# Performance work log

Measured on AMD Instinct MI355X. Metric: run time of the kernel, lower is better.

## Reference

```python
import jax, jax.numpy as jnp
import numpy as np

B, S, E = 2, 2048, 4096
H, KVH, D = 32, 8, 128          # query heads, kv heads, head_dim
GROUPS = H // KVH               # 4
WINDOW = 4096                   # sliding window (>= S -> fully causal)
ROPE_THETA = 10000.0


def _rope_sin_cos(position_ids):
    # inv_freq over even dims, freqs duplicated (Mixtral/GPT-NeoX style)
    inv_freq = 1.0 / (ROPE_THETA ** (jnp.arange(0, D, 2, dtype=jnp.float32) / D))  # [D/2]
    freqs = position_ids.astype(jnp.float32)[..., None] * inv_freq  # [B,S,D/2]
    emb = jnp.concatenate((freqs, freqs), axis=-1)                  # [B,S,D]
    # add head axis for broadcasting against [B,S,H,D]
    return jnp.sin(emb)[:, :, None, :], jnp.cos(emb)[:, :, None, :]


def _rotate_half(x):
    return jnp.concatenate((-x[..., D // 2:], x[..., :D // 2]), axis=-1)


def setup_inputs() -> dict:
    key = jax.random.key(0)
    ks = jax.random.split(key, 5)
    w_scale = 1.0 / np.sqrt(E)
    hidden_states = jax.random.normal(ks[0], (B, S, E), jnp.float32)
    Wq = jax.random.normal(ks[1], (E, H * D), jnp.float32) * w_scale
    Wk = jax.random.normal(ks[2], (E, KVH * D), jnp.float32) * w_scale
    Wv = jax.random.normal(ks[3], (E, KVH * D), jnp.float32) * w_scale
    Wo = jax.random.normal(ks[4], (H * D, E), jnp.float32) * w_scale
    # sliding-window causal mask: tril then zero entries more than WINDOW back
    causal = jnp.tril(jnp.ones((S, S), dtype=bool))
    causal = jnp.triu(causal, k=-WINDOW)[None, None]  # [1,1,S,S]
    attention_mask = jnp.ones((B, S), jnp.int32)
    position_ids = jnp.broadcast_to(jnp.arange(S, dtype=jnp.int32), (B, S))
    return dict(hidden_states=hidden_states, Wq=Wq, Wk=Wk, Wv=Wv, Wo=Wo,
                causal_mask=causal, attention_mask=attention_mask,
                position_ids=position_ids)


def reference(hidden_states, Wq, Wk, Wv, Wo, causal_mask, attention_mask, position_ids):
    # projections + head split
    q = (hidden_states @ Wq).reshape(B, S, H, D)
    k = (hidden_states @ Wk).reshape(B, S, KVH, D)
    v = (hidden_states @ Wv).reshape(B, S, KVH, D)

    # inline RoPE on q and k
    sin, cos = _rope_sin_cos(position_ids)
    q = q * cos + _rotate_half(q) * sin
    k = k * cos + _rotate_half(k) * sin

    # GQA: repeat kv heads to match query heads
    k = jnp.repeat(k, GROUPS, axis=2)  # [B,S,H,D]
    v = jnp.repeat(v, GROUPS, axis=2)

    # combined mask -> additive bias
    mask = causal_mask[:, :, :S, :S] & (attention_mask[:, None, None, :] > 0)  # [B|1,1,S,S]
    bias = jnp.where(mask, 0.0, jnp.finfo(jnp.float32).min)

    scores = jnp.einsum('bqhd,bkhd->bhqk', q, k) / jnp.sqrt(jnp.float32(D)) + bias
    probs = jax.nn.softmax(scores, axis=-1)
    attn = jnp.einsum('bhqk,bkhd->bqhd', probs, v).reshape(B, S, H * D)
    return attn @ Wo
```

## Files before the change

kernel.cpp:

```cpp
#include <hip/hip_runtime.h>
#include <hip/hip_bf16.h>
#include <cstdint>
#include <cstddef>

#define B_ 2
#define S_ 2048
#define E_ 4096
#define H_ 32
#define KVH_ 8
#define D_ 128
#define M_ (B_*S_)
#define HD_ (H_*D_)
#define KVD_ (KVH_*D_)
#define NQKV_ 6144

typedef unsigned short u16;
typedef __attribute__((ext_vector_type(8))) short bf16x8;
typedef __attribute__((ext_vector_type(4))) float f32x4;
typedef __attribute__((ext_vector_type(16))) float f32x16;

__device__ __forceinline__ float bf2f(u16 u) {
  union { float f; uint32_t i; } v; v.i = ((uint32_t)u) << 16; return v.f;
}
__device__ __forceinline__ u16 f2bf(float f) {
  union { float f; uint32_t i; } v; v.f = f;
  uint32_t r = v.i + 0x7FFF + ((v.i >> 16) & 1);
  return (u16)(r >> 16);
}

__device__ __forceinline__ void gload_lds16(const void* g, void* l) {
  __builtin_amdgcn_global_load_lds(
      (const __attribute__((address_space(1))) void*)g,
      (__attribute__((address_space(3))) void*)l, 16, 0, 0);
}

__global__ __launch_bounds__(256) void k_f2bf(const float* __restrict__ in,
                                              u16* __restrict__ out, int n) {
  int i = (blockIdx.x * 256 + threadIdx.x) * 4;
  if (i + 3 < n) {
    float4 v = *(const float4*)(in + i);
    *(ushort4*)(out + i) = make_ushort4(f2bf(v.x), f2bf(v.y), f2bf(v.z), f2bf(v.w));
  }
}

__global__ __launch_bounds__(256) void k_transpose_f2bf(const float* __restrict__ in,
                                                        u16* __restrict__ out, int R, int C) {
  __shared__ float tile[64][65];
  const int c0 = blockIdx.x * 64, r0 = blockIdx.y * 64;
  const int tid = threadIdx.x;
  const int lx = tid & 63, ty = tid >> 6;
#pragma unroll
  for (int i = 0; i < 16; ++i)
    tile[ty + 4 * i][lx] = in[(size_t)(r0 + ty + 4 * i) * C + c0 + lx];
  __syncthreads();
  const int oy = tid & 31, xb = tid >> 5;
#pragma unroll
  for (int i = 0; i < 8; ++i) {
    int X = xb + 8 * i;
    *(ushort2*)(out + (size_t)(c0 + X) * R + r0 + 2 * oy) =
        make_ushort2(f2bf(tile[2 * oy][X]), f2bf(tile[2 * oy + 1][X]));
  }
}

__global__ __launch_bounds__(256) void k_transpose_v(const u16* __restrict__ vlin,
                                                     u16* __restrict__ vt, int stride) {
  __shared__ u16 tile[64][65];
  const int bk = blockIdx.z;
  const int b = bk >> 3, kvh = bk & 7;
  const int s0 = blockIdx.x * 64, d0 = blockIdx.y * 64;
  const int tid = threadIdx.x;
  const int lx = tid & 63, ty = tid >> 6;
#pragma unroll
  for (int i = 0; i < 16; ++i)
    tile[ty + 4 * i][lx] =
        vlin[(size_t)(b * S_ + s0 + ty + 4 * i) * stride + kvh * D_ + d0 + lx];
  __syncthreads();
  const int oy = tid & 31, xb = tid >> 5;
#pragma unroll
  for (int i = 0; i < 8; ++i) {
    int X = xb + 8 * i;
    *(ushort2*)(vt + ((size_t)bk * D_ + d0 + X) * S_ + s0 + 2 * oy) =
        make_ushort2(tile[2 * oy][X], tile[2 * oy + 1][X]);
  }
}

__global__ __launch_bounds__(256) void k_table(float2* __restrict__ tab) {
  int i = blockIdx.x * 256 + threadIdx.x;
  if (i < S_ * 64) {
    int s = i >> 6, d = i & 63;
    float inv = powf(10000.0f, -(float)d / 64.0f);
    float f = (float)s * inv;
    tab[i] = make_float2(sinf(f), cosf(f));
  }
}

__global__ __launch_bounds__(256) void k_rope(const u16* __restrict__ in, u16* __restrict__ out,
                                              const float2* __restrict__ tab,
                                              const int* __restrict__ pos,
                                              int heads, int in_stride, int total) {
  int i = blockIdx.x * 256 + threadIdx.x;
  if (i >= total) return;
  int d = i & 63;
  int s = (i >> 6) & (S_ - 1);
  int bh = i >> 17;
  int h = bh % heads, b = bh / heads;
  size_t ibase = ((size_t)(b * S_ + s)) * in_stride + h * D_;
  float2 scv = tab[pos[b * S_ + s] * 64 + d];
  float x1 = bf2f(in[ibase + d]), x2 = bf2f(in[ibase + d + 64]);
  size_t obase = ((size_t)bh * S_ + s) * D_;
  out[obase + d]      = f2bf(x1 * scv.y - x2 * scv.x);
  out[obase + d + 64] = f2bf(x2 * scv.y + x1 * scv.x);
}

template<bool OUTF32>
__global__ __launch_bounds__(256) void k_gemm_bt(const u16* __restrict__ A,
                                                 const u16* __restrict__ BT,
                                                 void* __restrict__ Cp,
                                                 int M, int N, int K) {
  __shared__ __align__(16) u16 As[128 * 64];
  __shared__ __align__(16) u16 Bs[128 * 64];
  const int tid = threadIdx.x;
  const int wid = tid >> 6, lane = tid & 63;
  const int l32 = lane & 31, hi = lane >> 5;
  const int nbn = N >> 7;
  const int tm = blockIdx.x / nbn, tn = blockIdx.x % nbn;
  const int m0 = tm << 7, n0 = tn << 7;
  const int wr = wid >> 1, wc = wid & 1;

  f32x16 acc[2][2] = {};
  const int srow = (wid << 3) + (lane >> 3);
  const int sblk = lane & 7;

  for (int kt = 0; kt < K; kt += 64) {
#pragma unroll
    for (int c = 0; c < 4; ++c) {
      int r = (c << 5) + srow;
      int gb = sblk ^ (r & 7);
      gload_lds16(A  + (size_t)(m0 + r) * K + kt + (gb << 3), As + (c << 11) + (wid << 9));
      gload_lds16(BT + (size_t)(n0 + r) * K + kt + (gb << 3), Bs + (c << 11) + (wid << 9));
    }
    __syncthreads();
    bf16x8 af[2][4], bfr[2][4];
#pragma unroll
    for (int mi = 0; mi < 2; ++mi)
#pragma unroll
      for (int ks = 0; ks < 4; ++ks) {
        int ar = (wr << 6) + (mi << 5) + l32;
        int cb = (ks << 1) + hi;
        af[mi][ks] = *(const bf16x8*)(As + ar * 64 + ((cb ^ (ar & 7)) << 3));
      }
#pragma unroll
    for (int ni = 0; ni < 2; ++ni)
#pragma unroll
      for (int ks = 0; ks < 4; ++ks) {
        int br = (wc << 6) + (ni << 5) + l32;
        int cb = (ks << 1) + hi;
        bfr[ni][ks] = *(const bf16x8*)(Bs + br * 64 + ((cb ^ (br & 7)) << 3));
      }
#pragma unroll
    for (int ks = 0; ks < 4; ++ks)
#pragma unroll
      for (int mi = 0; mi < 2; ++mi)
#pragma unroll
        for (int ni = 0; ni < 2; ++ni)
          acc[mi][ni] = __builtin_amdgcn_mfma_f32_32x32x16_bf16(af[mi][ks], bfr[ni][ks],
                                                                acc[mi][ni], 0, 0, 0);
    __syncthreads();
  }

#pragma unroll
  for (int mi = 0; mi < 2; ++mi)
#pragma unroll
    for (int ni = 0; ni < 2; ++ni) {
      int col = n0 + (wc << 6) + (ni << 5) + l32;
#pragma unroll
      for (int r = 0; r < 16; ++r) {
        int row = m0 + (wr << 6) + (mi << 5) + (r & 3) + ((r >> 2) << 3) + (hi << 2);
        if (OUTF32) ((float*)Cp)[(size_t)row * N + col] = acc[mi][ni][r];
        else        ((u16*)Cp)[(size_t)row * N + col]  = f2bf(acc[mi][ni][r]);
      }
    }
}

__global__ __launch_bounds__(512, 4) void k_attn(const u16* __restrict__ QKV,
                                                 const u16* __restrict__ Kr,
                                                 const u16* __restrict__ Vt,
                                                 const float2* __restrict__ tab,
                                                 const int* __restrict__ pos,
                                                 u16* __restrict__ ctx) {
  __shared__ __align__(16) u16 Ks[2][64 * 128];
  __shared__ __align__(16) u16 Vs[2][128 * 64];
  __shared__ __align__(16) u16 Ps[8][16 * 40];
  const int bid = blockIdx.x;
  const int qt = 15 - (bid >> 6);
  const int bh = bid & 63;
  const int b = bh >> 5, h = bh & 31;
  const int kvh = h >> 2;
  const int tid = threadIdx.x;
  const int w = tid >> 6, lane = tid & 63;
  const int lrow = lane & 15, lk = lane >> 4;
  const int q0w = qt * 128 + w * 16;

  const int s = q0w + lrow;
  const int p = pos[b * S_ + s];
  const u16* q0 = QKV + ((size_t)(b * S_ + s)) * NQKV_ + h * D_ + lk * 8;
  bf16x8 raw[4];
#pragma unroll
  for (int ks = 0; ks < 4; ++ks) raw[ks] = *(const bf16x8*)(q0 + ks * 32);
  bf16x8 qf[4];
#pragma unroll
  for (int ks = 0; ks < 2; ++ks)
#pragma unroll
    for (int e = 0; e < 8; ++e) {
      int d = ks * 32 + lk * 8 + e;
      float2 scv = tab[p * 64 + d];
      float x1 = bf2f((u16)raw[ks][e]), x2 = bf2f((u16)raw[ks + 2][e]);
      qf[ks][e]     = (short)f2bf(x1 * scv.y - x2 * scv.x);
      qf[ks + 2][e] = (short)f2bf(x2 * scv.y + x1 * scv.x);
    }

  float m[4] = {-1e30f, -1e30f, -1e30f, -1e30f};
  float l[4] = {0.f, 0.f, 0.f, 0.f};
  f32x4 o[8] = {};

  const u16* kbase = Kr + (size_t)(b * KVH_ + kvh) * S_ * D_;
  const u16* vbase = Vt + (size_t)(b * KVH_ + kvh) * D_ * S_;
  const float cl = 0.12751743435f;
  const int nt = 2 * qt + 2;

  auto STAGE = [&](int buf, int kb) {
    const int kv0 = kb << 6;
#pragma unroll
    for (int c = 0; c < 2; ++c) {
      int r = w * 8 + (lane >> 4) + c * 4;
      gload_lds16(kbase + (size_t)(kv0 + r) * D_ + (((lane & 15) ^ (r & 7)) << 3),
                  &Ks[buf][(w * 8 + c * 4) * 128]);
    }
#pragma unroll
    for (int c = 0; c < 2; ++c) {
      int r = w * 16 + (lane >> 3) + c * 8;
      gload_lds16(vbase + (size_t)r * S_ + kv0 + (((lane & 7) ^ (r & 7)) << 3),
                  &Vs[buf][(w * 16 + c * 8) * 64]);
    }
  };

  STAGE(0, 0);
  int cur = 0;
  for (int kb = 0; kb < nt; ++kb) {
    __syncthreads();
    if (kb + 1 < nt) STAGE(cur ^ 1, kb + 1);
    const int kv0 = kb << 6;
    if (kv0 <= q0w + 15) {
      const u16* Kb = &Ks[cur][0];
      const u16* Vb = &Vs[cur][0];

      f32x4 sc[4] = {};
      __builtin_amdgcn_s_setprio(1);
#pragma unroll
      for (int n0 = 0; n0 < 4; ++n0) {
#pragma unroll
        for (int ks = 0; ks < 4; ++ks) {
          int krow = (n0 << 4) + lrow;
          bf16x8 kf = *(const bf16x8*)(Kb + krow * 128 + ((((ks << 2) + lk) ^ (krow & 7)) << 3));
          sc[n0] = __builtin_amdgcn_mfma_f32_16x16x32_bf16(qf[ks], kf, sc[n0], 0, 0, 0);
        }
      }
      __builtin_amdgcn_s_setprio(0);

      const bool diag = (kv0 + 63 > q0w);
      float mnew[4] = {m[0], m[1], m[2], m[3]};
#pragma unroll
      for (int n0 = 0; n0 < 4; ++n0)
#pragma unroll
        for (int j = 0; j < 4; ++j) {
          float v = sc[n0][j] * cl;
          if (diag && (kv0 + (n0 << 4) + lrow > q0w + (lk << 2) + j)) v = -1e30f;
          sc[n0][j] = v;
          mnew[j] = fmaxf(mnew[j], v);
        }
#pragma unroll
      for (int j = 0; j < 4; ++j) {
        float v = mnew[j];
        v = fmaxf(v, __shfl_xor(v, 1));
        v = fmaxf(v, __shfl_xor(v, 2));
        v = fmaxf(v, __shfl_xor(v, 4));
        v = fmaxf(v, __shfl_xor(v, 8));
        mnew[j] = v;
      }

      bool need = false;
#pragma unroll
      for (int j = 0; j < 4; ++j) need |= (mnew[j] - m[j] > 11.5f);
      if (__any(need)) {
        float alpha[4];
#pragma unroll
        for (int j = 0; j < 4; ++j) {
          alpha[j] = exp2f(m[j] - mnew[j]);
          m[j] = mnew[j];
          l[j] *= alpha[j];
        }
#pragma unroll
        for (int db = 0; db < 8; ++db)
#pragma unroll
          for (int j = 0; j < 4; ++j)
            o[db][j] *= alpha[j];
      }

      float rs[4] = {0.f, 0.f, 0.f, 0.f};
#pragma unroll
      for (int n0 = 0; n0 < 4; ++n0)
#pragma unroll
        for (int j = 0; j < 4; ++j) {
          float pv = exp2f(sc[n0][j] - m[j]);
          sc[n0][j] = pv;
          rs[j] += pv;
        }
#pragma unroll
      for (int j = 0; j < 4; ++j) {
        float v = rs[j];
        v += __shfl_xor(v, 1); v += __shfl_xor(v, 2);
        v += __shfl_xor(v, 4); v += __shfl_xor(v, 8);
        l[j] += v;
      }

      u16* pw = &Ps[w][0];
#pragma unroll
      for (int half = 0; half < 2; ++half) {
        asm volatile("s_waitcnt lgkmcnt(0)" ::: "memory");
#pragma unroll
        for (int n0 = 0; n0 < 2; ++n0)
#pragma unroll
          for (int j = 0; j < 4; ++j)
            pw[((lk << 2) + j) * 40 + (n0 << 4) + lrow] =
                f2bf(sc[(half << 1) + n0][j]);
        bf16x8 pf = *(const bf16x8*)(pw + lrow * 40 + (lk << 3));
        __builtin_amdgcn_s_setprio(1);
#pragma unroll
        for (int db = 0; db < 8; ++db) {
          int dr = (db << 4) + lrow;
          bf16x8 vf = *(const bf16x8*)(Vb + dr * 64 + ((((half << 2) + lk) ^ (dr & 7)) << 3));
          o[db] = __builtin_amdgcn_mfma_f32_16x16x32_bf16(pf, vf, o[db], 0, 0, 0);
        }
        __builtin_amdgcn_s_setprio(0);
      }
    }
    cur ^= 1;
  }

#pragma unroll
  for (int j = 0; j < 4; ++j) l[j] = 1.0f / l[j];
#pragma unroll
  for (int db = 0; db < 8; ++db)
#pragma unroll
    for (int j = 0; j < 4; ++j) {
      int q = q0w + (lk << 2) + j;
      ctx[((size_t)(b * S_ + q)) * HD_ + h * D_ + (db << 4) + lrow] = f2bf(o[db][j] * l[j]);
    }
}

extern "C" void kernel_launch(void* const* d_in, const int* in_sizes, int n_in,
                              void* d_out, int out_size, void* d_ws, size_t ws_size,
                              hipStream_t stream) {
  const float* hidden = (const float*)d_in[0];
  const float* Wq = (const float*)d_in[1];
  const float* Wk = (const float*)d_in[2];
  const float* Wv = (const float*)d_in[3];
  const float* Wo = (const float*)d_in[4];
  const int* pos_ids = (const int*)d_in[7];

  char* ws = (char*)d_ws;
  u16* hs      = (u16*)(ws);
  u16* ctx     = hs;
  u16* wqkvt   = (u16*)(ws + 33554432ull);
  u16* wot     = wqkvt;
  u16* qkvlin  = (u16*)(ws + 83886080ull);
  u16* kr      = (u16*)(ws + 134217728ull);
  u16* vt      = (u16*)(ws + 142606336ull);
  float2* tab  = (float2*)(ws + 150994944ull);

  k_f2bf<<<dim3((M_*E_)/1024), dim3(256), 0, stream>>>(hidden, hs, M_*E_);
  k_transpose_f2bf<<<dim3(HD_/64, E_/64), dim3(256), 0, stream>>>(Wq, wqkvt, E_, HD_);
  k_transpose_f2bf<<<dim3(KVD_/64, E_/64), dim3(256), 0, stream>>>(Wk, wqkvt + (size_t)HD_*E_, E_, KVD_);
  k_transpose_f2bf<<<dim3(KVD_/64, E_/64), dim3(256), 0, stream>>>(Wv, wqkvt + (size_t)(HD_+KVD_)*E_, E_, KVD_);
  k_gemm_bt<false><<<dim3((M_/128)*(NQKV_/128)), dim3(256), 0, stream>>>(hs, wqkvt, (void*)qkvlin, M_, NQKV_, E_);
  k_transpose_f2bf<<<dim3(E_/64, HD_/64), dim3(256), 0, stream>>>(Wo, wot, HD_, E_);
  k_table<<<dim3((S_*64)/256), dim3(256), 0, stream>>>(tab);
  k_rope<<<dim3((B_*KVH_*S_*64)/256), dim3(256), 0, stream>>>(qkvlin + HD_, kr, tab, pos_ids, KVH_, NQKV_, B_*KVH_*S_*64);
  k_transpose_v<<<dim3(S_/64, D_/64, B_*KVH_), dim3(256), 0, stream>>>(qkvlin + HD_ + KVD_, vt, NQKV_);
  k_attn<<<dim3(B_*H_*(S_/128)), dim3(512), 0, stream>>>(qkvlin, kr, vt, tab, pos_ids, ctx);
  k_gemm_bt<true><<<dim3((M_/128)*(E_/128)), dim3(256), 0, stream>>>(ctx, wot, d_out, M_, E_, HD_);
}
```

Before: 671.2 us.

## Replace GEMM with 256x256 tiled, double-buffered 8-wave pipelined kernel

Both projection GEMMs now use a new kernel with 256x256 output tiles, 8 waves per block and 16x16x32 MFMA. It double-buffers A/B tiles in LDS with fine-grained staged async loads, explicit vmcnt waits and raw barriers to overlap global loads with MFMA work, and raises wave priority around the MFMA bursts. The intent is to cut the load stalls and per-tile overhead of the old single-buffered 128x128 kernel. The larger tiles give fewer blocks (384 for QKV, 256 for output) and more register pressure, and the hand-tuned vmcnt accounting is fragile.

```diff
diff --git a/kernel.cpp b/kernel.cpp
--- a/kernel.cpp
+++ b/kernel.cpp
@@ -17,7 +17,6 @@
 typedef unsigned short u16;
 typedef __attribute__((ext_vector_type(8))) short bf16x8;
 typedef __attribute__((ext_vector_type(4))) float f32x4;
-typedef __attribute__((ext_vector_type(16))) float f32x16;
 
 __device__ __forceinline__ float bf2f(u16 u) {
   union { float f; uint32_t i; } v; v.i = ((uint32_t)u) << 16; return v.f;
@@ -33,6 +32,10 @@
       (const __attribute__((address_space(1))) void*)g,
       (__attribute__((address_space(3))) void*)l, 16, 0, 0);
 }
+
+#define FENCE() asm volatile("" ::: "memory")
+#define BARRIER() do { FENCE(); __builtin_amdgcn_s_barrier(); FENCE(); } while (0)
+#define VMCNT6() asm volatile("s_waitcnt vmcnt(6)" ::: "memory")
 
 __global__ __launch_bounds__(256) void k_f2bf(const float* __restrict__ in,
                                               u16* __restrict__ out, int n) {
@@ -113,71 +116,131 @@
 }
 
 template<bool OUTF32>
-__global__ __launch_bounds__(256) void k_gemm_bt(const u16* __restrict__ A,
-                                                 const u16* __restrict__ BT,
-                                                 void* __restrict__ Cp,
-                                                 int M, int N, int K) {
-  __shared__ __align__(16) u16 As[128 * 64];
-  __shared__ __align__(16) u16 Bs[128 * 64];
+__global__ __launch_bounds__(512, 2) void k_gemm8(const u16* __restrict__ A,
+                                                  const u16* __restrict__ BT,
+                                                  void* __restrict__ Cp,
+                                                  int M, int N, int K) {
+  __shared__ __align__(16) u16 L[8 * 8192];
   const int tid = threadIdx.x;
-  const int wid = tid >> 6, lane = tid & 63;
-  const int l32 = lane & 31, hi = lane >> 5;
-  const int nbn = N >> 7;
+  const int w = tid >> 6, lane = tid & 63;
+  const int lrow = lane & 15, lk = lane >> 4;
+  const int nbn = N >> 8;
   const int tm = blockIdx.x / nbn, tn = blockIdx.x % nbn;
-  const int m0 = tm << 7, n0 = tn << 7;
-  const int wr = wid >> 1, wc = wid & 1;
-
-  f32x16 acc[2][2] = {};
-  const int srow = (wid << 3) + (lane >> 3);
-  const int sblk = lane & 7;
-
-  for (int kt = 0; kt < K; kt += 64) {
-#pragma unroll
-    for (int c = 0; c < 4; ++c) {
-      int r = (c << 5) + srow;
-      int gb = sblk ^ (r & 7);
-      gload_lds16(A  + (size_t)(m0 + r) * K + kt + (gb << 3), As + (c << 11) + (wid << 9));
-      gload_lds16(BT + (size_t)(n0 + r) * K + kt + (gb << 3), Bs + (c << 11) + (wid << 9));
-    }
-    __syncthreads();
-    bf16x8 af[2][4], bfr[2][4];
-#pragma unroll
-    for (int mi = 0; mi < 2; ++mi)
-#pragma unroll
-      for (int ks = 0; ks < 4; ++ks) {
-        int ar = (wr << 6) + (mi << 5) + l32;
-        int cb = (ks << 1) + hi;
-        af[mi][ks] = *(const bf16x8*)(As + ar * 64 + ((cb ^ (ar & 7)) << 3));
-      }
-#pragma unroll
-    for (int ni = 0; ni < 2; ++ni)
-#pragma unroll
-      for (int ks = 0; ks < 4; ++ks) {
-        int br = (wc << 6) + (ni << 5) + l32;
-        int cb = (ks << 1) + hi;
-        bfr[ni][ks] = *(const bf16x8*)(Bs + br * 64 + ((cb ^ (br & 7)) << 3));
-      }
-#pragma unroll
-    for (int ks = 0; ks < 4; ++ks)
-#pragma unroll
-      for (int mi = 0; mi < 2; ++mi)
-#pragma unroll
-        for (int ni = 0; ni < 2; ++ni)
-          acc[mi][ni] = __builtin_amdgcn_mfma_f32_32x32x16_bf16(af[mi][ks], bfr[ni][ks],
-                                                                acc[mi][ni], 0, 0, 0);
-    __syncthreads();
-  }
-
-#pragma unroll
-  for (int mi = 0; mi < 2; ++mi)
-#pragma unroll
-    for (int ni = 0; ni < 2; ++ni) {
-      int col = n0 + (wc << 6) + (ni << 5) + l32;
-#pragma unroll
-      for (int r = 0; r < 16; ++r) {
-        int row = m0 + (wr << 6) + (mi << 5) + (r & 3) + ((r >> 2) << 3) + (hi << 2);
-        if (OUTF32) ((float*)Cp)[(size_t)row * N + col] = acc[mi][ni][r];
-        else        ((u16*)Cp)[(size_t)row * N + col]  = f2bf(acc[mi][ni][r]);
+  const int m0 = tm << 8, n0 = tn << 8;
+  const int wm = w >> 2, wn = w & 3;
+
+  f32x4 acc[8][4] = {};
+  bf16x8 bres[4][2];
+  const int nt = K >> 6;
+
+  const u16* RA[2] = { &L[(0 + wm) * 8192],       &L[(4 + wm) * 8192] };
+  const u16* RB[2] = { &L[(2 + (wn >> 1)) * 8192], &L[(6 + (wn >> 1)) * 8192] };
+
+  auto STAGE = [&](int buf, int mat, int half, int t) {
+    const u16* src = mat ? BT : A;
+    const int base0 = mat ? n0 : m0;
+    u16* reg = &L[(buf * 4 + mat * 2 + half) * 8192];
+#pragma unroll
+    for (int c = 0; c < 2; ++c) {
+      int rl = (c << 6) + (w << 3) + (lane >> 3);
+      int gb = (lane & 7) ^ (rl & 7);
+      gload_lds16(src + (size_t)(base0 + (half << 7) + rl) * K + (t << 6) + (gb << 3),
+                  reg + ((c << 6) + (w << 3)) * 64);
+    }
+  };
+  auto LDB = [&](int buf) {
+#pragma unroll
+    for (int nf = 0; nf < 4; ++nf)
+#pragma unroll
+      for (int ks = 0; ks < 2; ++ks) {
+        int br = ((wn & 1) << 6) + (nf << 4) + lrow;
+        int cb = (ks << 2) + lk;
+        bres[nf][ks] = *(const bf16x8*)(RB[buf] + br * 64 + ((cb ^ (br & 7)) << 3));
+      }
+  };
+  auto LDA2 = [&](int buf, int mp, bf16x8 (&af)[2][2]) {
+#pragma unroll
+    for (int d = 0; d < 2; ++d)
+#pragma unroll
+      for (int ks = 0; ks < 2; ++ks) {
+        int ar = (((mp << 1) + d) << 4) + lrow;
+        int cb = (ks << 2) + lk;
+        af[d][ks] = *(const bf16x8*)(RA[buf] + ar * 64 + ((cb ^ (ar & 7)) << 3));
+      }
+  };
+  auto MM2 = [&](int mp, bf16x8 (&af)[2][2]) {
+    __builtin_amdgcn_s_setprio(1);
+#pragma unroll
+    for (int ks = 0; ks < 2; ++ks)
+#pragma unroll
+      for (int d = 0; d < 2; ++d)
+#pragma unroll
+        for (int nf = 0; nf < 4; ++nf)
+          acc[(mp << 1) + d][nf] = __builtin_amdgcn_mfma_f32_16x16x32_bf16(
+              af[d][ks], bres[nf][ks], acc[(mp << 1) + d][nf], 0, 0, 0);
+    __builtin_amdgcn_s_setprio(0);
+  };
+
+  STAGE(0, 1, 0, 0); STAGE(0, 1, 1, 0);
+  STAGE(0, 0, 0, 0); STAGE(0, 0, 1, 0);
+  STAGE(1, 1, 0, 1); STAGE(1, 1, 1, 1);
+
+  const int niter = nt >> 1;
+  for (int i = 0; i < niter; ++i) {
+    const int t1 = 2 * i + 1;
+    const int t2 = (2 * i + 2 < nt) ? 2 * i + 2 : nt - 1;
+    const int t3 = (2 * i + 3 < nt) ? 2 * i + 3 : nt - 1;
+    bf16x8 afA[2][2], afB[2][2];
+
+    STAGE(1, 0, 0, t1);
+    VMCNT6();
+    BARRIER();
+    LDB(0); LDA2(0, 0, afA);
+    MM2(0, afA);
+    LDA2(0, 1, afB);
+    BARRIER();
+    STAGE(1, 0, 1, t1);
+    MM2(1, afB);
+    LDA2(0, 2, afA);
+    BARRIER();
+    STAGE(0, 1, 0, t2);
+    MM2(2, afA);
+    LDA2(0, 3, afB);
+    BARRIER();
+    STAGE(0, 1, 1, t2);
+    MM2(3, afB);
+    BARRIER();
+
+    STAGE(0, 0, 0, t2);
+    VMCNT6();
+    BARRIER();
+    LDB(1); LDA2(1, 0, afA);
+    MM2(0, afA);
+    LDA2(1, 1, afB);
+    BARRIER();
+    STAGE(0, 0, 1, t2);
+    MM2(1, afB);
+    LDA2(1, 2, afA);
+    BARRIER();
+    STAGE(1, 1, 0, t3);
+    MM2(2, afA);
+    LDA2(1, 3, afB);
+    BARRIER();
+    STAGE(1, 1, 1, t3);
+    MM2(3, afB);
+    BARRIER();
+  }
+
+#pragma unroll
+  for (int mi = 0; mi < 8; ++mi)
+#pragma unroll
+    for (int nf = 0; nf < 4; ++nf) {
+      int col = n0 + (wn << 6) + (nf << 4) + lrow;
+#pragma unroll
+      for (int j = 0; j < 4; ++j) {
+        int row = m0 + (wm << 7) + (mi << 4) + (lk << 2) + j;
+        if (OUTF32) ((float*)Cp)[(size_t)row * N + col] = acc[mi][nf][j];
+        else        ((u16*)Cp)[(size_t)row * N + col]  = f2bf(acc[mi][nf][j]);
       }
     }
 }
@@ -382,11 +445,11 @@
   k_transpose_f2bf<<<dim3(HD_/64, E_/64), dim3(256), 0, stream>>>(Wq, wqkvt, E_, HD_);
   k_transpose_f2bf<<<dim3(KVD_/64, E_/64), dim3(256), 0, stream>>>(Wk, wqkvt + (size_t)HD_*E_, E_, KVD_);
   k_transpose_f2bf<<<dim3(KVD_/64, E_/64), dim3(256), 0, stream>>>(Wv, wqkvt + (size_t)(HD_+KVD_)*E_, E_, KVD_);
-  k_gemm_bt<false><<<dim3((M_/128)*(NQKV_/128)), dim3(256), 0, stream>>>(hs, wqkvt, (void*)qkvlin, M_, NQKV_, E_);
+  k_gemm8<false><<<dim3((M_/256)*(NQKV_/256)), dim3(512), 0, stream>>>(hs, wqkvt, (void*)qkvlin, M_, NQKV_, E_);
   k_transpose_f2bf<<<dim3(E_/64, HD_/64), dim3(256), 0, stream>>>(Wo, wot, HD_, E_);
   k_table<<<dim3((S_*64)/256), dim3(256), 0, stream>>>(tab);
   k_rope<<<dim3((B_*KVH_*S_*64)/256), dim3(256), 0, stream>>>(qkvlin + HD_, kr, tab, pos_ids, KVH_, NQKV_, B_*KVH_*S_*64);
   k_transpose_v<<<dim3(S_/64, D_/64, B_*KVH_), dim3(256), 0, stream>>>(qkvlin + HD_ + KVD_, vt, NQKV_);
   k_attn<<<dim3(B_*H_*(S_/128)), dim3(512), 0, stream>>>(qkvlin, kr, vt, tab, pos_ids, ctx);
-  k_gemm_bt<true><<<dim3((M_/128)*(E_/128)), dim3(256), 0, stream>>>(ctx, wot, d_out, M_, E_, HD_);
-}
+  k_gemm8<true><<<dim3((M_/256)*(E_/256)), dim3(512), 0, stream>>>(ctx, wot, d_out, M_, E_, HD_);
+}
```

After: 587.4 us. 12.5% less time.
